# Kernel tuning notes

Measured on AMD Instinct MI355X. Metric: run time of the kernel, lower is better.

The kernel has to match this reference:

```python
import jax, jax.numpy as jnp
import numpy as np

SQRT_HALF = 0.7071067811865476
DILATIONS = [3 ** (i % 4) for i in range(8)]  # [1,3,9,27,1,3,9,27]


def conv1d(x, w, b, dilation=1):
    # x: [B, Cin, L], w: [Cout, Cin, K], 'same' padding
    out = jax.lax.conv_general_dilated(
        x, w, window_strides=(1,), padding='SAME',
        rhs_dilation=(dilation,),
        dimension_numbers=('NCH', 'OIH', 'NCH'))
    return out + b[None, :, None]


def encoder(x, enc_start_w, enc_start_b, glu_w, glu_b, enc_end_w, enc_end_b):
    # EncoderAny (eval mode -> dropout is identity)
    h = conv1d(x, enc_start_w, enc_start_b)                  # [B, mid, N]
    for i in range(len(DILATIONS)):
        g = conv1d(h, glu_w[i], glu_b[i], dilation=DILATIONS[i])  # [B, 2*mid, N]
        a, b = jnp.split(g, 2, axis=1)
        h = (h + a * jax.nn.sigmoid(b)) * SQRT_HALF           # GLU + residual
    out = conv1d(h, enc_end_w, enc_end_b)                     # [B, 2*d, N]
    K, V = jnp.split(out, 2, axis=1)                          # each [B, d, N]
    return K, V


def reference(in_s, in_t, c_t,
              enc_start_w, enc_start_b, glu_w, glu_b, enc_end_w, enc_end_b,
              wc_pre, w_pre, b_pre, wc_post, w_post, b_post):
    # ---- encoder: source -> K, V ----
    K_s, V_s = encoder(in_s, enc_start_w, enc_start_b, glu_w, glu_b,
                       enc_end_w, enc_end_b)                  # [B, d, N] each
    d = K_s.shape[1]

    # ---- pre-decoder: target + speaker code -> Q ----
    h_t = in_t + jnp.einsum('bc,cd->bd', c_t, wc_pre)[:, :, None]  # [B, D, T]
    Q_t = conv1d(h_t, w_pre, b_pre)                           # [B, d, T]

    # ---- custom attention: softmax over SOURCE axis (dim=1) ----
    scores = jnp.einsum('bdn,bdt->bnt', K_s, Q_t) / jnp.sqrt(
        jnp.asarray(d, dtype=K_s.dtype))                      # [B, N, T]
    A = jax.nn.softmax(scores, axis=1)                        # softmax over N
    R = jnp.einsum('bdn,bnt->bdt', V_s, A)                    # [B, d, T]

    # concat with Q (dropout p=0.9 in training; eval/deterministic -> identity)
    R = jnp.concatenate([R, Q_t], axis=1)                     # [B, 2d, T]

    # ---- post-decoder: attended features + speaker code -> y ----
    h_r = R + jnp.einsum('bc,cd->bd', c_t, wc_post)[:, :, None]
    y = conv1d(h_r, w_post, b_post)                           # [B, D, T]
    return y, A


def setup_inputs() -> dict:
    key = jax.random.key(0)
    ks = jax.random.split(key, 16)
    B, D, N, T = 16, 240, 2048, 2048
    mid, d, C = 512, 512, 8
    L = len(DILATIONS)

    def w(k, shape, fan_in):
        return (jax.random.normal(k, shape, dtype=jnp.float32)
                / jnp.sqrt(jnp.asarray(fan_in, jnp.float32)))

    return {
        'in_s': jax.random.normal(ks[0], (B, D, N), dtype=jnp.float32),
        'in_t': jax.random.normal(ks[1], (B, D, T), dtype=jnp.float32),
        'c_t': jax.random.normal(ks[2], (B, C), dtype=jnp.float32),
        'enc_start_w': w(ks[3], (mid, D, 1), D),
        'enc_start_b': jnp.zeros((mid,), jnp.float32),
        'glu_w': w(ks[4], (L, 2 * mid, mid, 5), mid * 5),
        'glu_b': jnp.zeros((L, 2 * mid), jnp.float32),
        'enc_end_w': w(ks[5], (2 * d, mid, 1), mid),
        'enc_end_b': jnp.zeros((2 * d,), jnp.float32),
        'wc_pre': w(ks[6], (C, D), C),
        'w_pre': w(ks[7], (d, D, 1), D),
        'b_pre': jnp.zeros((d,), jnp.float32),
        'wc_post': w(ks[8], (C, 2 * d), C),
        'w_post': w(ks[9], (D, 2 * d, 1), 2 * d),
        'b_post': jnp.zeros((D,), jnp.float32),
    }
```

## Files before the change

kernel.cpp:

```cpp
#include <hip/hip_runtime.h>
#include <cstdint>
#include <cstddef>

typedef unsigned short u16;
typedef __attribute__((ext_vector_type(8))) short short8;
typedef __attribute__((ext_vector_type(4))) float f32x4;

static constexpr int BB = 16, DIN = 240, NN = 2048, TT = 2048;
static constexpr long long Y_SIZE = (long long)BB * DIN * TT;
static constexpr float SQRT_HALF_F = 0.70710678118654752440f;
static constexpr int HPAD = 64;
static constexpr int HROWS = NN + 2 * HPAD;

#define DEVI __device__ __forceinline__

DEVI u16 f2bf(float f) {
    unsigned u = __builtin_bit_cast(unsigned, f);
    u += 0x7FFFu + ((u >> 16) & 1u);
    return (u16)(u >> 16);
}
DEVI float bf2f(u16 h) {
    unsigned u = ((unsigned)h) << 16;
    return __builtin_bit_cast(float, u);
}

DEVI void gld16(const void* g, const void* l) {
    __builtin_amdgcn_global_load_lds(
        (const __attribute__((address_space(1))) unsigned int*)g,
        (__attribute__((address_space(3))) unsigned int*)l, 16, 0, 0);
}

DEVI int glu_perm(int g) {
    int tile = g >> 8, r = g & 255;
    int wcq = r >> 6, r2 = r & 63;
    int n = r2 >> 4, fr = r2 & 15;
    return tile * 128 + wcq * 32 + (n >> 1) * 16 + fr + (n & 1) * 512;
}

struct GemmP {
    const u16* A; long long a_bstride; int lda;
    const u16* Bw; long long b_bstride; long long b_tapstride; int ldb;
    int ntaps; int shift0; int dshift; int Kt; int ks_log2;
    void* out; long long o_bstride; int ldc;
    const float* bias; int bias_bstride;
    float scale;
    int store_ncols;
};

#define FENCE() asm volatile("" ::: "memory")
#define SBAR()  do { FENCE(); __builtin_amdgcn_s_barrier(); FENCE(); } while (0)

template <int OUTK>
__global__ __launch_bounds__(512, 2)
void gemm256(GemmP p, int tilesM, int tilesN) {
    __shared__ __align__(16) u16 As[2][256 * 64];
    __shared__ __align__(16) u16 Bs[3][256 * 64];
    const int tid = threadIdx.x;
    const int lane = tid & 63;
    const int wv = tid >> 6;
    const int wr = wv >> 2, wcq = wv & 3;
    const int fr = lane & 15, fq = lane >> 4;

    const int nwg = gridDim.x;
    int widx = (blockIdx.x & 7) * (nwg >> 3) + (blockIdx.x >> 3);
    const int mt = widx % tilesM; widx /= tilesM;
    const int nt = widx % tilesN;
    const int bz = widx / tilesN;
    const int n0 = mt * 256, c0 = nt * 256;

    const int lda = p.lda, ldb = p.ldb;
    const u16* Abase = p.A + (long long)bz * p.a_bstride;
    const u16* Bbase = p.Bw + (long long)bz * p.b_bstride;
    const int kmask = (1 << p.ks_log2) - 1;
    const int tot = p.ntaps << p.ks_log2;

    f32x4 acc[8][4];
#pragma unroll
    for (int m = 0; m < 8; ++m)
#pragma unroll
        for (int n = 0; n < 4; ++n) acc[m][n] = (f32x4){0.f, 0.f, 0.f, 0.f};

    const int srow = lane >> 3, sslot = lane & 7;
    const int js = (sslot ^ srow) << 3;
    const int sr0 = wv * 16 + srow;
    const int wvB = wv * 1024;

    const long long sA8 = 8LL * lda, sAh = 128LL * lda;
    const long long sB8 = 8LL * ldb, sBh = 128LL * ldb;
    const long long dAtap = (long long)p.dshift * lda - (long long)kmask * 64;
    const long long dBtap = p.b_tapstride - (long long)kmask * 64;

    auto aAddr = [&](int t) -> const u16* {
        int tap = t >> p.ks_log2;
        return Abase + (long long)(n0 + p.shift0 + tap * p.dshift + sr0) * lda
               + ((t & kmask) << 6) + js;
    };
    auto bAddr = [&](int t) -> const u16* {
        int tap = t >> p.ks_log2;
        return Bbase + (long long)tap * p.b_tapstride
               + (long long)(c0 + sr0) * ldb + ((t & kmask) << 6) + js;
    };

    u16* uA = &As[0][wvB];

    u16* pB0 = &Bs[0][0];
    u16* pB1 = &Bs[1][0];
    u16* pB2 = &Bs[2][0];

    {
        const u16* a0 = aAddr(0);
        gld16(a0, uA);              gld16(a0 + sA8, uA + 512);
        gld16(a0 + sAh, uA + 8192); gld16(a0 + sAh + sA8, uA + 8192 + 512);
        const u16* b0 = bAddr(0);
        u16* d0 = pB0 + wvB;
        gld16(b0, d0);              gld16(b0 + sB8, d0 + 512);
        gld16(b0 + sBh, d0 + 8192); gld16(b0 + sBh + sB8, d0 + 8192 + 512);
        const u16* b1 = bAddr(1);
        u16* d1 = pB1 + wvB;
        gld16(b1, d1);              gld16(b1 + sB8, d1 + 512);
        gld16(b1 + sBh, d1 + 8192); gld16(b1 + sBh + sB8, d1 + 8192 + 512);
    }
    const u16* aP = aAddr(1);
    const u16* bP = bAddr(2);
    asm volatile("s_waitcnt vmcnt(4)" ::: "memory");
    __builtin_amdgcn_s_barrier();
    FENCE();

    const int aoff0 = (wr * 128 + fr) * 64 + ((fq ^ (fr & 7)) << 3);
    const int aoff1 = (wr * 128 + fr) * 64 + (((4 + fq) ^ (fr & 7)) << 3);
    const int boff0 = (wcq * 64 + fr) * 64 + ((fq ^ (fr & 7)) << 3);
    const int boff1 = (wcq * 64 + fr) * 64 + (((4 + fq) ^ (fr & 7)) << 3);

    short8 af0[4][2], af1[4][2], bf0[2][2], bf1[2][2];

#define READ_AQ(DEST, MQ)                                                      \
    _Pragma("unroll")                                                          \
    for (int mi = 0; mi < 4; ++mi) {                                           \
        DEST[mi][0] = *(const short8*)&Ab[aoff0 + ((MQ) * 64 + mi * 16) * 64]; \
        DEST[mi][1] = *(const short8*)&Ab[aoff1 + ((MQ) * 64 + mi * 16) * 64]; \
    }
#define READ_BQ(BF, NQ)                                                        \
    _Pragma("unroll")                                                          \
    for (int ni = 0; ni < 2; ++ni) {                                           \
        BF[ni][0] = *(const short8*)&Bb[boff0 + ((NQ) * 32 + ni * 16) * 64];   \
        BF[ni][1] = *(const short8*)&Bb[boff1 + ((NQ) * 32 + ni * 16) * 64];   \
    }
#define MFMA_Q2(MQ, NQ, AF, BF)                                                \
    __builtin_amdgcn_s_setprio(1);                                             \
    _Pragma("unroll")                                                          \
    for (int mi = 0; mi < 4; ++mi) {                                           \
        _Pragma("unroll")                                                      \
        for (int ni = 0; ni < 2; ++ni) {                                       \
            _Pragma("unroll")                                                  \
            for (int kk = 0; kk < 2; ++kk)                                     \
                acc[(MQ) * 4 + mi][(NQ) * 2 + ni] =                            \
                    __builtin_amdgcn_mfma_f32_16x16x32_bf16(                   \
                        AF[mi][kk], BF[ni][kk],                                \
                        acc[(MQ) * 4 + mi][(NQ) * 2 + ni], 0, 0, 0);           \
        }                                                                      \
    }                                                                          \
    __builtin_amdgcn_s_setprio(0)

#define TILEBODY(BUF_, BRD_, BST_, DO_A_, DO_B_, STEPA_, STEPB_, VM_)          \
  {                                                                            \
    const u16* Ab = &As[BUF_][0];                                              \
    const u16* Bb = (BRD_);                                                    \
    u16* bDst = (BST_) + wvB;                                                  \
    READ_AQ(af0, 0);                                                           \
    READ_BQ(bf0, 0);                                                           \
    READ_BQ(bf1, 1);                                                           \
    if (DO_A_) { gld16(aP, uA + ((BUF_) ^ 1) * 16384);                         \
                 gld16(aP + sA8, uA + ((BUF_) ^ 1) * 16384 + 512); }           \
    MFMA_Q2(0, 0, af0, bf0);                                                   \
    READ_AQ(af1, 1);                                                           \
    if (DO_A_) { gld16(aP + sAh, uA + ((BUF_) ^ 1) * 16384 + 8192);            \
                 gld16(aP + sAh + sA8, uA + ((BUF_) ^ 1) * 16384 + 8192 + 512);\
                 aP += (STEPA_); }                                             \
    MFMA_Q2(0, 1, af0, bf1);                                                   \
    if (DO_B_) { gld16(bP, bDst);                                              \
                 gld16(bP + sB8, bDst + 512); }                                \
    MFMA_Q2(1, 1, af1, bf1);                                                   \
    if (DO_B_) { gld16(bP + sBh, bDst + 8192);                                 \
                 gld16(bP + sBh + sB8, bDst + 8192 + 512);                     \
                 bP += (STEPB_); }                                             \
    MFMA_Q2(1, 0, af1, bf0);                                                   \
    if ((VM_) == 4) asm volatile("s_waitcnt vmcnt(4)" ::: "memory");           \
    else if ((VM_) == 0) asm volatile("s_waitcnt vmcnt(0)" ::: "memory");      \
    SBAR();                                                                    \
  }

    int t = 0;
    for (; t + 3 < tot; t += 2) {
        const long long stA1 = (((t + 2) & kmask) != 0) ? 64 : dAtap;
        const long long stA2 = (((t + 3) & kmask) != 0) ? 64 : dAtap;
        const long long stB1 = (((t + 3) & kmask) != 0) ? 64 : dBtap;
        const long long stB2 = (((t + 4) & kmask) != 0) ? 64 : dBtap;
        TILEBODY(0, pB0, pB2, 1, 1, stA1, stB1, 4);
        TILEBODY(1, pB1, pB0, 1, 1, stA2, stB2, 4);
        u16* tmpB = pB0; pB0 = pB2; pB2 = pB1; pB1 = tmpB;
    }
    TILEBODY(0, pB0, pB2, 1, 0, 0, 0, 0);
    TILEBODY(1, pB1, pB0, 0, 0, 0, 0, -1);
#undef READ_AQ
#undef READ_BQ
#undef MFMA_Q2
#undef TILEBODY

    if constexpr (OUTK == 4) {
        const float* bp = p.bias;
#pragma unroll
        for (int m = 0; m < 8; ++m) {
#pragma unroll
            for (int pr = 0; pr < 2; ++pr) {
                int ca = c0 + wcq * 64 + (2 * pr) * 16 + fr;
                int chan = (c0 >> 1) + wcq * 32 + pr * 16 + fr;
                float biasa = bp[ca], biasb = bp[ca + 16];
#pragma unroll
                for (int r = 0; r < 4; ++r) {
                    int row = n0 + wr * 128 + m * 16 + fq * 4 + r;
                    float a = acc[m][2 * pr][r] + biasa;
                    float bq = acc[m][2 * pr + 1][r] + biasb;
                    float sig = 1.f / (1.f + __expf(-bq));
                    float h = bf2f(Abase[(long long)row * lda + chan]);
                    ((u16*)p.out)[(long long)bz * p.o_bstride + (long long)row * p.ldc + chan]
                        = f2bf((h + a * sig) * SQRT_HALF_F);
                }
            }
        }
        return;
    } else if constexpr (OUTK == 2) {
        const float* bias = p.bias + (long long)bz * p.bias_bstride;
#pragma unroll
        for (int m = 0; m < 8; ++m) {
#pragma unroll
            for (int n = 0; n < 4; ++n) {
                int col = c0 + wcq * 64 + n * 16 + fr;
                if (col >= p.store_ncols) continue;
                float cb = bias[col];
#pragma unroll
                for (int r = 0; r < 4; ++r) {
                    int row = n0 + wr * 128 + m * 16 + fq * 4 + r;
                    ((float*)p.out)[(long long)bz * p.o_bstride + (long long)col * p.ldc + row]
                        = acc[m][n][r] * p.scale + cb;
                }
            }
        }
        return;
    } else {
        const float* bias = p.bias ? p.bias + (long long)bz * p.bias_bstride : nullptr;
#pragma unroll
        for (int m = 0; m < 8; ++m) {
#pragma unroll
            for (int n = 0; n < 4; ++n) {
                int col = c0 + wcq * 64 + n * 16 + fr;
                float cb = (OUTK == 1 && bias) ? bias[col] : 0.f;
#pragma unroll
                for (int r = 0; r < 4; ++r) {
                    int row = n0 + wr * 128 + m * 16 + fq * 4 + r;
                    float v = acc[m][n][r] * p.scale + cb;
                    if (OUTK == 5) v += bias[row];
                    ((u16*)p.out)[(long long)bz * p.o_bstride + (long long)row * p.ldc + col]
                        = f2bf(v);
                }
            }
        }
    }
}


__global__ void cvt_glu(const float* src, u16* dst) {
    int u = blockIdx.x * 256 + threadIdx.x;
    if (u >= 8 * 1024 * 512) return;
    int i = u & 511;
    int o = (u >> 9) & 1023;
    int l = u >> 19;
    int hi = o >> 9;
    int op = o & 511;
    int tile = op >> 7;
    int wcq = (op >> 5) & 3;
    int nhalf = (op >> 4) & 1;
    int fr = op & 15;
    int g = tile * 256 + wcq * 64 + (2 * nhalf + hi) * 16 + fr;
    const float* s = src + (long long)u * 5;
    long long dbase = ((long long)l * 5 * 1024 + g) * 512 + i;
#pragma unroll
    for (int k = 0; k < 5; ++k)
        dst[dbase + (long long)k * 1024 * 512] = f2bf(s[k]);
}

__global__ void perm_bias(const float* gb, float* biasP) {
    int t = blockIdx.x * 256 + threadIdx.x;
    if (t >= 8 * 1024) return;
    int g = t & 1023, l = t >> 10;
    biasP[t] = gb[l * 1024 + glu_perm(g)];
}

__global__ void cvt_all(const float* enc_start_w, const float* enc_end_w,
                        const float* w_pre, const float* w_post,
                        u16* wstart, u16* wend, u16* wpre, u16* wpost) {
    int t = blockIdx.x * 256 + threadIdx.x;
    if (t < 131072) {
        int i = t & 255, o = t >> 8;
        wstart[t] = f2bf(i < 240 ? enc_start_w[o * 240 + i] : 0.f);
    } else if (t < 655360) {
        int q = t - 131072;
        wend[q] = f2bf(enc_end_w[q]);
    } else if (t < 786432) {
        int q = t - 655360;
        int i = q & 255, o = q >> 8;
        wpre[q] = f2bf(i < 240 ? w_pre[o * 240 + i] : 0.f);
    } else if (t < 1048576) {
        int q = t - 786432;
        int i = q & 1023, o = q >> 10;
        wpost[q] = f2bf(o < 240 ? w_post[o * 1024 + i] : 0.f);
    }
}

__global__ void transpose_in(const float* in_s, const float* in_t, u16* XS, u16* XT) {
    __shared__ float tile[32][33];
    int zz = blockIdx.z;
    const float* src = (zz < BB) ? in_s : in_t;
    u16* dst = (zz < BB) ? XS : XT;
    int b = zz & (BB - 1);
    int n0 = blockIdx.x * 32, c0 = blockIdx.y * 32;
    int tx = threadIdx.x, ty = threadIdx.y;
    int c = c0 + ty, n = n0 + tx;
    float v = 0.f;
    if (c < 240) v = src[((long long)b * 240 + c) * 2048 + n];
    tile[ty][tx] = v;
    __syncthreads();
    dst[((long long)b * 2048 + (n0 + ty)) * 256 + (c0 + tx)] = f2bf(tile[tx][ty]);
}

__global__ void zero_pads(u16* h0, u16* h1) {
    long long t = (long long)blockIdx.x * blockDim.x + threadIdx.x;
    const long long half = (long long)BB * 128 * 512;
    if (t >= 2 * half) return;
    u16* h = (t < half) ? h0 : h1;
    long long q = (t < half) ? t : t - half;
    int c = (int)(q % 512); long long r = q / 512;
    int rr = (int)(r % 128); int b = (int)(r / 128);
    int row = rr < HPAD ? rr : (HROWS - 128 + rr);
    h[((long long)b * HROWS + row) * 512 + c] = 0;
}

__global__ void bias_kernel(const float* ct,
                            const float* wcpre, const float* wpre_f, const float* bpre,
                            const float* wcpost, const float* wpost_f, const float* bpost,
                            float* qbias, float* ybias) {
    __shared__ float s[1024];
    int b = blockIdx.x; int tid = threadIdx.x;
    if (blockIdx.y == 0) {
        if (tid < 240) {
            float a = 0.f;
            for (int c = 0; c < 8; ++c) a += ct[b * 8 + c] * wcpre[c * 240 + tid];
            s[tid] = a;
        }
        __syncthreads();
        for (int o = tid; o < 512; o += 256) {
            float a = bpre[o];
            for (int d0 = 0; d0 < 240; ++d0) a += wpre_f[o * 240 + d0] * s[d0];
            qbias[b * 512 + o] = a;
        }
    } else {
        for (int e = tid; e < 1024; e += 256) {
            float a = 0.f;
            for (int c = 0; c < 8; ++c) a += ct[b * 8 + c] * wcpost[c * 1024 + e];
            s[e] = a;
        }
        __syncthreads();
        if (tid < 240) {
            float a = bpost[tid];
            for (int e = 0; e < 1024; ++e) a += wpost_f[tid * 1024 + e] * s[e];
            ybias[b * 240 + tid] = a;
        }
    }
}

__global__ __launch_bounds__(256)
void softmax_rows(const u16* St, u16* AT) {
    int b = blockIdx.y;
    int t = blockIdx.x * 4 + (threadIdx.x >> 6);
    int lane = threadIdx.x & 63;
    const u16* row = St + ((long long)b * TT + t) * NN;
    short8 v[4];
#pragma unroll
    for (int i = 0; i < 4; ++i) v[i] = ((const short8*)row)[i * 64 + lane];
    float f[32];
#pragma unroll
    for (int i = 0; i < 4; ++i)
#pragma unroll
        for (int j = 0; j < 8; ++j) f[i * 8 + j] = bf2f((u16)v[i][j]);
    float m = -3.4e38f;
#pragma unroll
    for (int i = 0; i < 32; ++i) m = fmaxf(m, f[i]);
#pragma unroll
    for (int s = 1; s < 64; s <<= 1) m = fmaxf(m, __shfl_xor(m, s, 64));
    float sum = 0.f;
#pragma unroll
    for (int i = 0; i < 32; ++i) { f[i] = __expf(f[i] - m); sum += f[i]; }
#pragma unroll
    for (int s = 1; s < 64; s <<= 1) sum += __shfl_xor(sum, s, 64);
    float li = 1.f / sum;
    u16* atrow = AT + ((long long)b * TT + t) * NN;
#pragma unroll
    for (int i = 0; i < 4; ++i) {
        short8 pk;
#pragma unroll
        for (int j = 0; j < 8; ++j) pk[j] = (short)f2bf(f[i * 8 + j] * li);
        ((short8*)atrow)[i * 64 + lane] = pk;
    }
}

__global__ void transpose_out(const u16* AT, float* A) {
    __shared__ float tile[32][33];
    int b = blockIdx.z;
    int n0 = blockIdx.x * 32, t0 = blockIdx.y * 32;
    int tx = threadIdx.x, ty = threadIdx.y;
#pragma unroll
    for (int k = 0; k < 4; ++k) {
        int t = t0 + ty + k * 8;
        tile[ty + k * 8][tx] = bf2f(AT[((long long)b * TT + t) * NN + n0 + tx]);
    }
    __syncthreads();
#pragma unroll
    for (int k = 0; k < 4; ++k) {
        int n = n0 + ty + k * 8;
        A[((long long)b * NN + n) * TT + t0 + tx] = tile[tx][ty + k * 8];
    }
}


extern "C" void kernel_launch(void* const* d_in, const int* in_sizes, int n_in,
                              void* d_out, int out_size, void* d_ws, size_t ws_size,
                              hipStream_t stream) {
    const float* in_s        = (const float*)d_in[0];
    const float* in_t        = (const float*)d_in[1];
    const float* c_t         = (const float*)d_in[2];
    const float* enc_start_w = (const float*)d_in[3];
    const float* enc_start_b = (const float*)d_in[4];
    const float* glu_w       = (const float*)d_in[5];
    const float* glu_b       = (const float*)d_in[6];
    const float* enc_end_w   = (const float*)d_in[7];
    const float* enc_end_b   = (const float*)d_in[8];
    const float* wc_pre      = (const float*)d_in[9];
    const float* w_pre       = (const float*)d_in[10];
    const float* b_pre       = (const float*)d_in[11];
    const float* wc_post     = (const float*)d_in[12];
    const float* w_post      = (const float*)d_in[13];
    const float* b_post      = (const float*)d_in[14];

    char* w = (char*)d_ws;
    u16* wglu   = (u16*)w; w += 8LL * 5 * 1024 * 512 * 2;
    u16* wstart = (u16*)w; w += 512LL * 256 * 2;
    u16* wend   = (u16*)w; w += 1024LL * 512 * 2;
    u16* wpre   = (u16*)w; w += 512LL * 256 * 2;
    u16* wpost  = (u16*)w; w += 256LL * 1024 * 2;
    u16* XS     = (u16*)w; w += (long long)BB * NN * 256 * 2;
    u16* XT     = (u16*)w; w += (long long)BB * TT * 256 * 2;
    u16* h0     = (u16*)w; w += (long long)BB * HROWS * 512 * 2;
    u16* h1     = (u16*)w; w += (long long)BB * HROWS * 512 * 2;
    u16* Kb     = (u16*)w; w += (long long)BB * NN * 512 * 2;
    u16* Vb     = (u16*)w; w += (long long)BB * 512 * NN * 2;
    u16* Rc     = (u16*)w; w += (long long)BB * TT * 1024 * 2;
    u16* ATb    = (u16*)w; w += (long long)BB * TT * NN * 2;
    float* qbias = (float*)w; w += 16LL * 512 * 4;
    float* ybias = (float*)w; w += 16LL * 256 * 4;
    float* biasP = (float*)w; w += 8LL * 1024 * 4;
    if ((size_t)(w - (char*)d_ws) > ws_size) return;

    float* yout = (float*)d_out;
    float* Areg = yout + Y_SIZE;
    u16* Sbf = (u16*)Areg;

    cvt_glu<<<(8 * 1024 * 512) / 256, 256, 0, stream>>>(glu_w, wglu);
    perm_bias<<<(8 * 1024 + 255) / 256, 256, 0, stream>>>(glu_b, biasP);
    cvt_all<<<1048576 / 256, 256, 0, stream>>>(enc_start_w, enc_end_w, w_pre, w_post,
                                               wstart, wend, wpre, wpost);
    transpose_in<<<dim3(NN / 32, 256 / 32, 2 * BB), dim3(32, 32), 0, stream>>>(in_s, in_t, XS, XT);
    zero_pads<<<(2LL * BB * 128 * 512 + 255) / 256, 256, 0, stream>>>(h0, h1);
    bias_kernel<<<dim3(16, 2), 256, 0, stream>>>(c_t, wc_pre, w_pre, b_pre,
                                                 wc_post, w_post, b_post, qbias, ybias);

    {
        GemmP p{}; p.A = XS; p.a_bstride = (long long)NN * 256; p.lda = 256;
        p.Bw = wstart; p.b_bstride = 0; p.b_tapstride = 0; p.ldb = 256;
        p.ntaps = 1; p.shift0 = 0; p.dshift = 0; p.Kt = 256; p.ks_log2 = 2;
        p.out = h0 + HPAD * 512; p.o_bstride = (long long)HROWS * 512; p.ldc = 512;
        p.bias = enc_start_b; p.bias_bstride = 0; p.scale = 1.f; p.store_ncols = 512;
        gemm256<1><<<8 * 2 * 16, 512, 0, stream>>>(p, 8, 2);
    }

    const int dils[8] = {1, 3, 9, 27, 1, 3, 9, 27};
    u16* hin = h0; u16* hout = h1;
    for (int l = 0; l < 8; ++l) {
        GemmP q{}; q.A = hin + HPAD * 512; q.a_bstride = (long long)HROWS * 512; q.lda = 512;
        q.Bw = wglu + (long long)l * 5 * 1024 * 512; q.b_bstride = 0;
        q.b_tapstride = 1024LL * 512; q.ldb = 512;
        q.ntaps = 5; q.shift0 = -2 * dils[l]; q.dshift = dils[l]; q.Kt = 512; q.ks_log2 = 3;
        q.out = hout + HPAD * 512; q.o_bstride = (long long)HROWS * 512; q.ldc = 512;
        q.bias = biasP + l * 1024; q.bias_bstride = 0; q.scale = 1.f; q.store_ncols = 1024;
        gemm256<4><<<8 * 4 * 16, 512, 0, stream>>>(q, 8, 4);
        u16* tmp = hin; hin = hout; hout = tmp;
    }

    {
        GemmP p{}; p.A = hin + HPAD * 512; p.a_bstride = (long long)HROWS * 512; p.lda = 512;
        p.Bw = wend; p.b_bstride = 0; p.b_tapstride = 0; p.ldb = 512;
        p.ntaps = 1; p.shift0 = 0; p.dshift = 0; p.Kt = 512; p.ks_log2 = 3;
        p.out = Kb; p.o_bstride = (long long)NN * 512; p.ldc = 512;
        p.bias = enc_end_b; p.bias_bstride = 0; p.scale = 1.f; p.store_ncols = 512;
        gemm256<1><<<8 * 2 * 16, 512, 0, stream>>>(p, 8, 2);
    }
    {
        GemmP p{}; p.A = wend + 512LL * 512; p.a_bstride = 0; p.lda = 512;
        p.Bw = hin + HPAD * 512; p.b_bstride = (long long)HROWS * 512; p.b_tapstride = 0; p.ldb = 512;
        p.ntaps = 1; p.shift0 = 0; p.dshift = 0; p.Kt = 512; p.ks_log2 = 3;
        p.out = Vb; p.o_bstride = 512LL * NN; p.ldc = NN;
        p.bias = enc_end_b + 512; p.bias_bstride = 0; p.scale = 1.f; p.store_ncols = NN;
        gemm256<5><<<2 * 8 * 16, 512, 0, stream>>>(p, 2, 8);
    }

    {
        GemmP p{}; p.A = XT; p.a_bstride = (long long)TT * 256; p.lda = 256;
        p.Bw = wpre; p.b_bstride = 0; p.b_tapstride = 0; p.ldb = 256;
        p.ntaps = 1; p.shift0 = 0; p.dshift = 0; p.Kt = 256; p.ks_log2 = 2;
        p.out = Rc + 512; p.o_bstride = (long long)TT * 1024; p.ldc = 1024;
        p.bias = qbias; p.bias_bstride = 512; p.scale = 1.f; p.store_ncols = 512;
        gemm256<1><<<8 * 2 * 16, 512, 0, stream>>>(p, 8, 2);
    }

    {
        GemmP p{}; p.A = Rc + 512; p.a_bstride = (long long)TT * 1024; p.lda = 1024;
        p.Bw = Kb; p.b_bstride = (long long)NN * 512; p.b_tapstride = 0; p.ldb = 512;
        p.ntaps = 1; p.shift0 = 0; p.dshift = 0; p.Kt = 512; p.ks_log2 = 3;
        p.out = Sbf; p.o_bstride = (long long)TT * NN; p.ldc = NN;
        p.bias = nullptr; p.bias_bstride = 0; p.scale = 0.04419417382415922f;
        p.store_ncols = NN;
        gemm256<1><<<8 * 8 * 16, 512, 0, stream>>>(p, 8, 8);
    }

    softmax_rows<<<dim3(TT / 4, BB), 256, 0, stream>>>(Sbf, ATb);
    transpose_out<<<dim3(NN / 32, TT / 32, BB), dim3(32, 8), 0, stream>>>(ATb, Areg);

    {
        GemmP p{}; p.A = ATb; p.a_bstride = (long long)TT * NN; p.lda = NN;
        p.Bw = Vb; p.b_bstride = 512LL * NN; p.b_tapstride = 0; p.ldb = NN;
        p.ntaps = 1; p.shift0 = 0; p.dshift = 0; p.Kt = NN; p.ks_log2 = 5;
        p.out = Rc; p.o_bstride = (long long)TT * 1024; p.ldc = 1024;
        p.bias = nullptr; p.bias_bstride = 0; p.scale = 1.f; p.store_ncols = 512;
        gemm256<1><<<8 * 2 * 16, 512, 0, stream>>>(p, 8, 2);
    }

    {
        GemmP p{}; p.A = Rc; p.a_bstride = (long long)TT * 1024; p.lda = 1024;
        p.Bw = wpost; p.b_bstride = 0; p.b_tapstride = 0; p.ldb = 1024;
        p.ntaps = 1; p.shift0 = 0; p.dshift = 0; p.Kt = 1024; p.ks_log2 = 4;
        p.out = yout; p.o_bstride = (long long)DIN * TT; p.ldc = TT;
        p.bias = ybias; p.bias_bstride = 240; p.scale = 1.f; p.store_ncols = 240;
        gemm256<2><<<8 * 1 * 16, 512, 0, stream>>>(p, 8, 1);
    }
}
```

Baseline: 1.639 ms.

## Add 256x128 tile GLU GEMM kernel with BK=32 triple-buffered pipeline

Replaces the 256x256-tile GLU dilated-conv GEMM with a dedicated kernel using 256x128 output tiles, K-step 32, and triple-buffered LDS for both A and B, launched with twice as many workgroups. It updates the weight and bias permutation to match the narrower tile's gated-channel interleaving. The smaller tile lowers register and LDS use, allowing more workgroups per CU and better CU coverage. In exchange it raises per-output A-tile reloads and adds more barriers per K-step.

```diff
diff --git a/kernel.cpp b/kernel.cpp
--- a/kernel.cpp
+++ b/kernel.cpp
@@ -31,10 +31,10 @@
 }
 
 DEVI int glu_perm(int g) {
-    int tile = g >> 8, r = g & 255;
-    int wcq = r >> 6, r2 = r & 63;
+    int tile = g >> 7, r = g & 127;
+    int wc2 = (r >> 6) & 1, r2 = r & 63;
     int n = r2 >> 4, fr = r2 & 15;
-    return tile * 128 + wcq * 32 + (n >> 1) * 16 + fr + (n & 1) * 512;
+    return tile * 64 + wc2 * 32 + (n >> 1) * 16 + fr + (n & 1) * 512;
 }
 
 struct GemmP {
@@ -102,7 +102,6 @@
     };
 
     u16* uA = &As[0][wvB];
-
     u16* pB0 = &Bs[0][0];
     u16* pB1 = &Bs[1][0];
     u16* pB2 = &Bs[2][0];
@@ -206,29 +205,7 @@
 #undef MFMA_Q2
 #undef TILEBODY
 
-    if constexpr (OUTK == 4) {
-        const float* bp = p.bias;
-#pragma unroll
-        for (int m = 0; m < 8; ++m) {
-#pragma unroll
-            for (int pr = 0; pr < 2; ++pr) {
-                int ca = c0 + wcq * 64 + (2 * pr) * 16 + fr;
-                int chan = (c0 >> 1) + wcq * 32 + pr * 16 + fr;
-                float biasa = bp[ca], biasb = bp[ca + 16];
-#pragma unroll
-                for (int r = 0; r < 4; ++r) {
-                    int row = n0 + wr * 128 + m * 16 + fq * 4 + r;
-                    float a = acc[m][2 * pr][r] + biasa;
-                    float bq = acc[m][2 * pr + 1][r] + biasb;
-                    float sig = 1.f / (1.f + __expf(-bq));
-                    float h = bf2f(Abase[(long long)row * lda + chan]);
-                    ((u16*)p.out)[(long long)bz * p.o_bstride + (long long)row * p.ldc + chan]
-                        = f2bf((h + a * sig) * SQRT_HALF_F);
-                }
-            }
-        }
-        return;
-    } else if constexpr (OUTK == 2) {
+    if constexpr (OUTK == 2) {
         const float* bias = p.bias + (long long)bz * p.bias_bstride;
 #pragma unroll
         for (int m = 0; m < 8; ++m) {
@@ -267,6 +244,136 @@
     }
 }
 
+__global__ __launch_bounds__(512, 4)
+void gemm128glu(GemmP p, int tilesM, int tilesN) {
+    __shared__ __align__(16) u16 As[3][256 * 32];
+    __shared__ __align__(16) u16 Bs[3][128 * 32];
+    const int tid = threadIdx.x;
+    const int lane = tid & 63;
+    const int wv = tid >> 6;
+    const int wr4 = wv >> 1, wc2 = wv & 1;
+    const int fr = lane & 15, fq = lane >> 4;
+
+    const int nwg = gridDim.x;
+    int widx = (blockIdx.x & 7) * (nwg >> 3) + (blockIdx.x >> 3);
+    const int mt = widx % tilesM; widx /= tilesM;
+    const int nt = widx % tilesN;
+    const int bz = widx / tilesN;
+    const int n0 = mt * 256, c0 = nt * 128;
+
+    const int lda = p.lda, ldb = p.ldb;
+    const u16* Abase = p.A + (long long)bz * p.a_bstride;
+    const u16* Bbase = p.Bw;
+    const int kmask = (1 << p.ks_log2) - 1;
+    const int tot = p.ntaps << p.ks_log2;
+
+    f32x4 acc[4][4];
+#pragma unroll
+    for (int m = 0; m < 4; ++m)
+#pragma unroll
+        for (int n = 0; n < 4; ++n) acc[m][n] = (f32x4){0.f, 0.f, 0.f, 0.f};
+
+    const int srow = lane >> 2, sslot = lane & 3;
+    const int js = (sslot ^ (srow & 3)) << 3;
+    const int sr0 = wv * 16 + srow;
+    const long long sAh = 128LL * lda;
+    const long long dAtap = (long long)p.dshift * lda - (long long)kmask * 32;
+    const long long dBtap = p.b_tapstride - (long long)kmask * 32;
+
+    auto aAddr = [&](int t) -> const u16* {
+        int tap = t >> p.ks_log2;
+        return Abase + (long long)(n0 + p.shift0 + tap * p.dshift + sr0) * lda
+               + ((t & kmask) << 5) + js;
+    };
+    auto bAddr = [&](int t) -> const u16* {
+        int tap = t >> p.ks_log2;
+        return Bbase + (long long)tap * p.b_tapstride
+               + (long long)(c0 + sr0) * ldb + ((t & kmask) << 5) + js;
+    };
+
+    const int wv512 = wv * 512;
+    u16* pA0 = &As[0][0]; u16* pA1 = &As[1][0]; u16* pA2 = &As[2][0];
+    u16* pB0 = &Bs[0][0]; u16* pB1 = &Bs[1][0]; u16* pB2 = &Bs[2][0];
+
+    {
+        const u16* a0 = aAddr(0);
+        gld16(a0, pA0 + wv512); gld16(a0 + sAh, pA0 + wv512 + 4096);
+        const u16* b0 = bAddr(0);
+        gld16(b0, pB0 + wv512);
+        const u16* a1 = aAddr(1);
+        gld16(a1, pA1 + wv512); gld16(a1 + sAh, pA1 + wv512 + 4096);
+        const u16* b1 = bAddr(1);
+        gld16(b1, pB1 + wv512);
+    }
+    const u16* aP = aAddr(2);
+    const u16* bP = bAddr(2);
+    asm volatile("s_waitcnt vmcnt(0)" ::: "memory");
+    __builtin_amdgcn_s_barrier();
+    FENCE();
+
+    const int aoffb = (wr4 * 64 + fr) * 32 + ((fq ^ (fr & 3)) << 3);
+    const int boffb = (wc2 * 64 + fr) * 32 + ((fq ^ (fr & 3)) << 3);
+
+#define T128BODY(T_, DO_, VM_)                                                 \
+  {                                                                            \
+    const u16* Ab = pA0;                                                       \
+    const u16* Bb = pB0;                                                       \
+    short8 af[4], bf[4];                                                       \
+    _Pragma("unroll")                                                          \
+    for (int mi = 0; mi < 4; ++mi) af[mi] = *(const short8*)&Ab[aoffb + mi * 512]; \
+    _Pragma("unroll")                                                          \
+    for (int ni = 0; ni < 4; ++ni) bf[ni] = *(const short8*)&Bb[boffb + ni * 512]; \
+    if (DO_) {                                                                 \
+        gld16(aP, pA2 + wv512);                                                \
+        gld16(aP + sAh, pA2 + wv512 + 4096);                                   \
+        gld16(bP, pB2 + wv512);                                                \
+        long long stA = ((((T_) + 3) & kmask) != 0) ? 32 : dAtap;              \
+        long long stB = ((((T_) + 3) & kmask) != 0) ? 32 : dBtap;              \
+        aP += stA; bP += stB;                                                  \
+    }                                                                          \
+    __builtin_amdgcn_s_setprio(1);                                             \
+    _Pragma("unroll")                                                          \
+    for (int mi = 0; mi < 4; ++mi)                                             \
+        _Pragma("unroll")                                                      \
+        for (int ni = 0; ni < 4; ++ni)                                         \
+            acc[mi][ni] = __builtin_amdgcn_mfma_f32_16x16x32_bf16(             \
+                af[mi], bf[ni], acc[mi][ni], 0, 0, 0);                         \
+    __builtin_amdgcn_s_setprio(0);                                             \
+    if ((VM_) == 3) asm volatile("s_waitcnt vmcnt(3)" ::: "memory");           \
+    else if ((VM_) == 0) asm volatile("s_waitcnt vmcnt(0)" ::: "memory");      \
+    SBAR();                                                                    \
+    u16* tA = pA0; pA0 = pA1; pA1 = pA2; pA2 = tA;                             \
+    u16* tB = pB0; pB0 = pB1; pB1 = pB2; pB2 = tB;                             \
+  }
+
+    int t = 0;
+    for (; t < tot - 2; ++t) T128BODY(t, 1, 3);
+    T128BODY(t, 0, 0);
+    T128BODY(t, 0, -1);
+#undef T128BODY
+
+    const float* bp = p.bias;
+#pragma unroll
+    for (int m = 0; m < 4; ++m) {
+#pragma unroll
+        for (int pr = 0; pr < 2; ++pr) {
+            int ca = c0 + wc2 * 64 + (2 * pr) * 16 + fr;
+            int chan = (c0 >> 1) + wc2 * 32 + pr * 16 + fr;
+            float biasa = bp[ca], biasb = bp[ca + 16];
+#pragma unroll
+            for (int r = 0; r < 4; ++r) {
+                int row = n0 + wr4 * 64 + m * 16 + fq * 4 + r;
+                float a = acc[m][2 * pr][r] + biasa;
+                float bq = acc[m][2 * pr + 1][r] + biasb;
+                float sig = 1.f / (1.f + __expf(-bq));
+                float h = bf2f(Abase[(long long)row * lda + chan]);
+                ((u16*)p.out)[(long long)bz * p.o_bstride + (long long)row * p.ldc + chan]
+                    = f2bf((h + a * sig) * SQRT_HALF_F);
+            }
+        }
+    }
+}
+
 
 __global__ void cvt_glu(const float* src, u16* dst) {
     int u = blockIdx.x * 256 + threadIdx.x;
@@ -276,11 +383,11 @@
     int l = u >> 19;
     int hi = o >> 9;
     int op = o & 511;
-    int tile = op >> 7;
-    int wcq = (op >> 5) & 3;
+    int tile = op >> 6;
+    int wc2i = (op >> 5) & 1;
     int nhalf = (op >> 4) & 1;
     int fr = op & 15;
-    int g = tile * 256 + wcq * 64 + (2 * nhalf + hi) * 16 + fr;
+    int g = tile * 128 + wc2i * 64 + (2 * nhalf + hi) * 16 + fr;
     const float* s = src + (long long)u * 5;
     long long dbase = ((long long)l * 5 * 1024 + g) * 512 + i;
 #pragma unroll
@@ -497,10 +604,10 @@
         GemmP q{}; q.A = hin + HPAD * 512; q.a_bstride = (long long)HROWS * 512; q.lda = 512;
         q.Bw = wglu + (long long)l * 5 * 1024 * 512; q.b_bstride = 0;
         q.b_tapstride = 1024LL * 512; q.ldb = 512;
-        q.ntaps = 5; q.shift0 = -2 * dils[l]; q.dshift = dils[l]; q.Kt = 512; q.ks_log2 = 3;
+        q.ntaps = 5; q.shift0 = -2 * dils[l]; q.dshift = dils[l]; q.Kt = 512; q.ks_log2 = 4;
         q.out = hout + HPAD * 512; q.o_bstride = (long long)HROWS * 512; q.ldc = 512;
         q.bias = biasP + l * 1024; q.bias_bstride = 0; q.scale = 1.f; q.store_ncols = 1024;
-        gemm256<4><<<8 * 4 * 16, 512, 0, stream>>>(q, 8, 4);
+        gemm128glu<<<8 * 8 * 16, 512, 0, stream>>>(q, 8, 8);
         u16* tmp = hin; hin = hout; hout = tmp;
     }
 
```

New measurement: 1.816 ms. 1.11x slower.
